# Kernel tuning notes

Measured on AMD Instinct MI355X. Metric: run time of the kernel, lower is better.

## Reference

```python
import jax, jax.numpy as jnp
import numpy as np

N_HEAD = 16
EPS = 1e-6

def setup_inputs() -> dict:
    key = jax.random.key(0)
    ks = jax.random.split(key, 5)
    B, S, D = 2, 2048, 1024
    scale = 0.02
    return {
        "hidden_states": jax.random.normal(ks[0], (B, S, D), dtype=jnp.float32),
        "w_q": jax.random.normal(ks[1], (D, D), dtype=jnp.float32) * scale,
        "w_k": jax.random.normal(ks[2], (D, D), dtype=jnp.float32) * scale,
        "w_v": jax.random.normal(ks[3], (D, D), dtype=jnp.float32) * scale,
        "w_o": jax.random.normal(ks[4], (D, D), dtype=jnp.float32) * scale,
        "qk_norm_factor": jnp.float32(1.0 / np.sqrt(D // N_HEAD)),
    }

def reference(hidden_states, w_q, w_k, w_v, w_o, qk_norm_factor):
    B, S, D = hidden_states.shape
    H = N_HEAD
    hd = D // H
    # projections (torch Linear without bias: x @ W^T)
    q = jnp.einsum('bsd,ed->bse', hidden_states, w_q).reshape(B, S, H, hd).transpose(0, 2, 1, 3)
    k = jnp.einsum('bsd,ed->bse', hidden_states, w_k).reshape(B, S, H, hd).transpose(0, 2, 1, 3)
    v = jnp.einsum('bsd,ed->bse', hidden_states, w_v).reshape(B, S, H, hd).transpose(0, 2, 1, 3)
    # hypersphere (QK) normalization
    q = q / (jnp.linalg.norm(q, axis=-1, keepdims=True) + EPS)
    k = k / (jnp.linalg.norm(k, axis=-1, keepdims=True) + EPS)
    # scores [B,H,S,S], learned scale
    scores = jnp.einsum('bhqd,bhkd->bhqk', q, k) * qk_norm_factor
    causal = jnp.tril(jnp.ones((S, S), dtype=bool))
    scores = jnp.where(causal[None, None], scores, jnp.float32(-jnp.inf))
    probs = jax.nn.softmax(scores, axis=-1)
    attn = jnp.einsum('bhqk,bhkd->bhqd', probs, v)
    attn = attn.transpose(0, 2, 1, 3).reshape(B, S, D)
    out = jnp.einsum('bsd,ed->bse', attn, w_o)
    return out
```

## Files before the change

kernel.cpp:

```cpp
#include <hip/hip_runtime.h>
#include <hip/hip_bf16.h>

typedef __attribute__((ext_vector_type(8))) short short8;
typedef __attribute__((ext_vector_type(4))) float floatx4;

union BF8 { short8 v; __hip_bfloat16 b[8]; };
union BF4U { ushort4 u; __hip_bfloat16 b[4]; };

__device__ __forceinline__ short8 load8(const __hip_bfloat16* p) {
    return *reinterpret_cast<const short8*>(p);
}

__device__ __forceinline__ void storeC(float* p, float v) { *p = v; }
__device__ __forceinline__ void storeC(__hip_bfloat16* p, float v) { *p = __float2bfloat16(v); }

__device__ __forceinline__ unsigned pack_bf16(float a, float b) {
    unsigned ua = __float_as_uint(a) + 0x8000u;
    unsigned ub = __float_as_uint(b) + 0x8000u;
    return __builtin_amdgcn_perm(ub, ua, 0x07060302u);
}

__device__ __forceinline__ float exp2_fast(float x) {
#if __has_builtin(__builtin_amdgcn_exp2f)
    return __builtin_amdgcn_exp2f(x);
#else
    return __expf(x * 0.6931471805599453f);
#endif
}

__device__ __forceinline__ void gload_lds16(const __hip_bfloat16* g, __hip_bfloat16* l) {
    __builtin_amdgcn_global_load_lds(
        (const __attribute__((address_space(1))) void*)g,
        (__attribute__((address_space(3))) void*)l, 16, 0, 0);
}

__global__ __launch_bounds__(256) void cast_all(const float* __restrict__ hs,
                                                const float* __restrict__ wq,
                                                const float* __restrict__ wk,
                                                const float* __restrict__ wv,
                                                const float* __restrict__ wo,
                                                __hip_bfloat16* __restrict__ Xb,
                                                __hip_bfloat16* __restrict__ Wb) {
    int i = blockIdx.x * 256 + threadIdx.x;
    const float* src;
    __hip_bfloat16* dst;
    if (blockIdx.y == 0) {
        src = hs; dst = Xb;
    } else {
        int m = i >> 18;
        src = (m == 0) ? wq : (m == 1) ? wk : (m == 2) ? wv : wo;
        src -= (size_t)m * 1048576;
        dst = Wb;
    }
    float4 v = reinterpret_cast<const float4*>(src)[i];
    BF4U u;
    u.b[0] = __float2bfloat16(v.x);
    u.b[1] = __float2bfloat16(v.y);
    u.b[2] = __float2bfloat16(v.z);
    u.b[3] = __float2bfloat16(v.w);
    reinterpret_cast<ushort4*>(dst)[i] = u.u;
}

template <typename OutT>
__global__ __launch_bounds__(256) void gemm_bt(const __hip_bfloat16* __restrict__ A,
                                               const __hip_bfloat16* __restrict__ B0,
                                               OutT* __restrict__ C0,
                                               int N, int Kd,
                                               size_t zsB, size_t zsC,
                                               int normz, const float* __restrict__ scale_p) {
    __shared__ __hip_bfloat16 lA[128 * 32];
    __shared__ __hip_bfloat16 lB[128 * 32];
    const __hip_bfloat16* B = B0 + zsB * blockIdx.z;
    OutT* C = C0 + zsC * blockIdx.z;
    const int t = threadIdx.x;
    const int m0 = blockIdx.x * 128, n0 = blockIdx.y * 128;
    const int w = t >> 6, l = t & 63;
    const int wr = (w >> 1) * 64, wc = (w & 1) * 64;
    const int lr = l & 15, lq = l >> 4;

    const floatx4 zero4 = {0.f, 0.f, 0.f, 0.f};
    floatx4 acc[4][4];
#pragma unroll
    for (int mt = 0; mt < 4; ++mt)
#pragma unroll
        for (int nt = 0; nt < 4; ++nt) acc[mt][nt] = zero4;

    for (int k0 = 0; k0 < Kd; k0 += 32) {
#pragma unroll
        for (int i = 0; i < 2; ++i) {
            int flat = t + i * 256;
            int row = flat >> 2, ch = flat & 3;
            gload_lds16(A + (size_t)(m0 + row) * Kd + k0 + ch * 8, lA + flat * 8);
            gload_lds16(B + (size_t)(n0 + row) * Kd + k0 + ch * 8, lB + flat * 8);
        }
        __syncthreads();
        short8 af[4], bfr[4];
#pragma unroll
        for (int mt = 0; mt < 4; ++mt)
            af[mt] = load8(lA + (wr + mt * 16 + lr) * 32 + lq * 8);
#pragma unroll
        for (int nt = 0; nt < 4; ++nt)
            bfr[nt] = load8(lB + (wc + nt * 16 + lr) * 32 + lq * 8);
#pragma unroll
        for (int mt = 0; mt < 4; ++mt)
#pragma unroll
            for (int nt = 0; nt < 4; ++nt)
                acc[mt][nt] = __builtin_amdgcn_mfma_f32_16x16x32_bf16(
                    af[mt], bfr[nt], acc[mt][nt], 0, 0, 0);
        __syncthreads();
    }

    if (normz && blockIdx.z < 2) {
        const float fac = (blockIdx.z == 0) ? (*scale_p * 1.44269504f) : 1.0f;
#pragma unroll
        for (int mt = 0; mt < 4; ++mt)
#pragma unroll
            for (int r = 0; r < 4; ++r) {
                float ss = 0.f;
#pragma unroll
                for (int nt = 0; nt < 4; ++nt) {
                    float v = acc[mt][nt][r];
                    ss += v * v;
                }
                ss += __shfl_xor(ss, 1, 64);
                ss += __shfl_xor(ss, 2, 64);
                ss += __shfl_xor(ss, 4, 64);
                ss += __shfl_xor(ss, 8, 64);
                float inv = fac / (sqrtf(ss) + 1e-6f);
#pragma unroll
                for (int nt = 0; nt < 4; ++nt) acc[mt][nt][r] *= inv;
            }
    }

#pragma unroll
    for (int mt = 0; mt < 4; ++mt)
#pragma unroll
        for (int nt = 0; nt < 4; ++nt)
#pragma unroll
            for (int r = 0; r < 4; ++r) {
                int row = m0 + wr + mt * 16 + lq * 4 + r;
                int col = n0 + wc + nt * 16 + lr;
                storeC(C + (size_t)row * N + col, acc[mt][nt][r]);
            }
}

__global__ __launch_bounds__(256) void transpose_v(const __hip_bfloat16* __restrict__ V,
                                                   __hip_bfloat16* __restrict__ Vt) {
    const int S = 2048, D = 1024;
    __shared__ __hip_bfloat16 tile[64][72];
    int t = threadIdx.x;
    int s0 = blockIdx.x * 64;
    int bh = blockIdx.y, b = bh >> 4, h = bh & 15;
    const __hip_bfloat16* src = V + ((size_t)b * S) * D + h * 64;
#pragma unroll
    for (int i = 0; i < 2; ++i) {
        int flat = t + i * 256;
        int sr = flat >> 3, ch = flat & 7;
        *reinterpret_cast<short8*>(&tile[sr][ch * 8]) =
            load8(src + (size_t)(s0 + sr) * D + ch * 8);
    }
    __syncthreads();
    __hip_bfloat16* dst = Vt + (size_t)bh * 64 * S;
#pragma unroll
    for (int i = 0; i < 2; ++i) {
        int flat = t + i * 256;
        int d = flat >> 3, sc = flat & 7;
        BF8 u;
#pragma unroll
        for (int j = 0; j < 8; ++j) u.b[j] = tile[sc * 8 + j][d];
        *reinterpret_cast<short8*>(dst + (size_t)d * S + s0 + sc * 8) = u.v;
    }
}

__global__ __launch_bounds__(256) void flash_attn(const __hip_bfloat16* __restrict__ Q,
                                                  const __hip_bfloat16* __restrict__ K,
                                                  const __hip_bfloat16* __restrict__ Vt,
                                                  __hip_bfloat16* __restrict__ O) {
    const int S = 2048, D = 1024;
    __shared__ __align__(16) char smem[20480];
    const int t = threadIdx.x;
    const int w = t >> 6, l = t & 63;
    const int lr = l & 15, lq = l >> 4;
    const int id = blockIdx.x, jj = id >> 3;
    const int bh = (id & 7) * 4 + (jj & 3);
    const int jq = 31 - (jj >> 2);
    const int b = bh >> 4, h = bh & 15;
    const int q0 = jq * 64;
    const __hip_bfloat16* Qb = Q + ((size_t)b * S) * D + h * 64;
    const __hip_bfloat16* Kb = K + ((size_t)b * S) * D + h * 64;
    const __hip_bfloat16* Vb = Vt + (size_t)bh * 64 * S;
    __hip_bfloat16* lPw = reinterpret_cast<__hip_bfloat16*>(smem) + w * (64 * 40);

    short8 bq[4][2];
#pragma unroll
    for (int nt = 0; nt < 4; ++nt)
#pragma unroll
        for (int kt = 0; kt < 2; ++kt)
            bq[nt][kt] = load8(Qb + (size_t)(q0 + nt * 16 + lr) * D + kt * 32 + lq * 8);

    const floatx4 zero4 = {0.f, 0.f, 0.f, 0.f};
    floatx4 oacc[4][4];
    float lsum[4] = {0.f, 0.f, 0.f, 0.f};
#pragma unroll
    for (int mt = 0; mt < 4; ++mt)
#pragma unroll
        for (int nt = 0; nt < 4; ++nt) oacc[mt][nt] = zero4;

    auto body = [&](int k0, bool domask) {
        short8 bk[2][2], bv[4];
#pragma unroll
        for (int mt = 0; mt < 2; ++mt)
#pragma unroll
            for (int kt = 0; kt < 2; ++kt)
                bk[mt][kt] = load8(Kb + (size_t)(k0 + mt * 16 + lr) * D + kt * 32 + lq * 8);
#pragma unroll
        for (int nt = 0; nt < 4; ++nt)
            bv[nt] = load8(Vb + (size_t)(nt * 16 + lr) * S + k0 + lq * 8);
        floatx4 sacc[2][4];
#pragma unroll
        for (int mt = 0; mt < 2; ++mt)
#pragma unroll
            for (int nt = 0; nt < 4; ++nt) sacc[mt][nt] = zero4;
#pragma unroll
        for (int mt = 0; mt < 2; ++mt)
#pragma unroll
            for (int nt = 0; nt < 4; ++nt)
#pragma unroll
                for (int kt = 0; kt < 2; ++kt)
                    sacc[mt][nt] = __builtin_amdgcn_mfma_f32_16x16x32_bf16(
                        bk[mt][kt], bq[nt][kt], sacc[mt][nt], 0, 0, 0);
#pragma unroll
        for (int mt = 0; mt < 2; ++mt)
#pragma unroll
            for (int nt = 0; nt < 4; ++nt) {
                float p0 = exp2_fast(sacc[mt][nt][0]);
                float p1 = exp2_fast(sacc[mt][nt][1]);
                float p2 = exp2_fast(sacc[mt][nt][2]);
                float p3 = exp2_fast(sacc[mt][nt][3]);
                if (domask) {
                    const int qg = q0 + nt * 16 + lr;
                    const int kb = k0 + mt * 16 + lq * 4;
                    p0 = (kb + 0 <= qg) ? p0 : 0.f;
                    p1 = (kb + 1 <= qg) ? p1 : 0.f;
                    p2 = (kb + 2 <= qg) ? p2 : 0.f;
                    p3 = (kb + 3 <= qg) ? p3 : 0.f;
                }
                lsum[nt] += (p0 + p1) + (p2 + p3);
                uint2 d;
                d.x = pack_bf16(p0, p1);
                d.y = pack_bf16(p2, p3);
                *reinterpret_cast<uint2*>(lPw + (nt * 16 + lr) * 40 + mt * 16 + lq * 4) = d;
            }
        asm volatile("s_waitcnt lgkmcnt(0)" ::: "memory");
        short8 ap[4];
#pragma unroll
        for (int mtq = 0; mtq < 4; ++mtq)
            ap[mtq] = load8(lPw + (mtq * 16 + lr) * 40 + lq * 8);
#pragma unroll
        for (int mtq = 0; mtq < 4; ++mtq)
#pragma unroll
            for (int ntd = 0; ntd < 4; ++ntd)
                oacc[mtq][ntd] = __builtin_amdgcn_mfma_f32_16x16x32_bf16(
                    ap[mtq], bv[ntd], oacc[mtq][ntd], 0, 0, 0);
    };

    int ks = w;
    for (; ks < 2 * jq; ks += 4) body(ks * 32, false);
    for (; ks <= 2 * jq + 1; ks += 4) body(ks * 32, true);

#pragma unroll
    for (int nt = 0; nt < 4; ++nt) {
        float s = lsum[nt];
        s += __shfl_xor(s, 16, 64);
        s += __shfl_xor(s, 32, 64);
        lsum[nt] = s;
    }

    float* buf = reinterpret_cast<float*>(smem);
    const int row = t >> 2, c0 = (t & 3) * 4;
    __hip_bfloat16* Ob = O + ((size_t)b * S) * D + h * 64;
    float inv = 0.f;
#pragma unroll
    for (int chunk = 0; chunk < 4; ++chunk) {
#pragma unroll
        for (int mtq = 0; mtq < 4; ++mtq)
#pragma unroll
            for (int r = 0; r < 4; ++r)
                buf[w * 1280 + (mtq * 16 + lq * 4 + r) * 20 + lr] = oacc[mtq][chunk][r];
        if (chunk == 0 && lq == 0) {
#pragma unroll
            for (int nt = 0; nt < 4; ++nt)
                buf[w * 1280 + (nt * 16 + lr) * 20 + 16] = lsum[nt];
        }
        __syncthreads();
        if (chunk == 0) {
            float Lt = buf[row * 20 + 16] + buf[1280 + row * 20 + 16] +
                       buf[2560 + row * 20 + 16] + buf[3840 + row * 20 + 16];
            inv = 1.f / Lt;
        }
        float4 a = {0.f, 0.f, 0.f, 0.f};
#pragma unroll
        for (int w2 = 0; w2 < 4; ++w2) {
            float4 v = *reinterpret_cast<const float4*>(buf + w2 * 1280 + row * 20 + c0);
            a.x += v.x; a.y += v.y; a.z += v.z; a.w += v.w;
        }
        uint2 d;
        d.x = pack_bf16(a.x * inv, a.y * inv);
        d.y = pack_bf16(a.z * inv, a.w * inv);
        *reinterpret_cast<uint2*>(Ob + (size_t)(q0 + row) * D + chunk * 16 + c0) = d;
        if (chunk < 3) __syncthreads();
    }
}

extern "C" void kernel_launch(void* const* d_in, const int* in_sizes, int n_in,
                              void* d_out, int out_size, void* d_ws, size_t ws_size,
                              hipStream_t stream) {
    const float* hs  = (const float*)d_in[0];
    const float* wq  = (const float*)d_in[1];
    const float* wk  = (const float*)d_in[2];
    const float* wv  = (const float*)d_in[3];
    const float* wo  = (const float*)d_in[4];
    const float* qkf = (const float*)d_in[5];

    char* ws = (char*)d_ws;
    const size_t MB = 1024 * 1024;
    __hip_bfloat16* Xb  = (__hip_bfloat16*)(ws);
    __hip_bfloat16* Wqb = (__hip_bfloat16*)(ws + 8 * MB);
    __hip_bfloat16* Wob = (__hip_bfloat16*)(ws + 14 * MB);
    __hip_bfloat16* Qb  = (__hip_bfloat16*)(ws + 16 * MB);
    __hip_bfloat16* Vb  = (__hip_bfloat16*)(ws + 32 * MB);
    __hip_bfloat16* Vt  = (__hip_bfloat16*)(ws + 40 * MB);
    __hip_bfloat16* Ab  = (__hip_bfloat16*)(ws + 48 * MB);
    __hip_bfloat16* Kb  = (__hip_bfloat16*)(ws + 24 * MB);

    cast_all<<<dim3(4096, 2), 256, 0, stream>>>(hs, wq, wk, wv, wo, Xb, Wqb);

    gemm_bt<__hip_bfloat16><<<dim3(32, 8, 3), 256, 0, stream>>>(
        Xb, Wqb, Qb, 1024, 1024, (size_t)1048576, (size_t)4194304, 1, qkf);

    transpose_v<<<dim3(32, 32), 256, 0, stream>>>(Vb, Vt);
    flash_attn<<<1024, 256, 0, stream>>>(Qb, Kb, Vt, Ab);

    gemm_bt<float><<<dim3(32, 8, 1), 256, 0, stream>>>(
        Ab, Wob, (float*)d_out, 1024, 1024, (size_t)0, (size_t)0, 0, qkf);
}
```

Baseline: 197.3 us.

## Pair causal query tiles per block and prefetch next K/V fragments

Each flash-attention block now handles two query tiles, a long one (31-pr) and a short one (pr), so every block does the same amount of causal work. This halves the grid to 512 blocks. The key loop is also software-pipelined: the next iteration's K and V fragments are loaded into registers before the current tile's MFMAs run, hiding global load latency. In exchange it raises register pressure, adds an extra sync per chunk, and leaves fewer blocks to hide latency.

```diff
diff --git a/kernel.cpp b/kernel.cpp
--- a/kernel.cpp
+++ b/kernel.cpp
@@ -181,134 +181,166 @@
     const int t = threadIdx.x;
     const int w = t >> 6, l = t & 63;
     const int lr = l & 15, lq = l >> 4;
-    const int id = blockIdx.x, jj = id >> 3;
-    const int bh = (id & 7) * 4 + (jj & 3);
-    const int jq = 31 - (jj >> 2);
+    const int id = blockIdx.x;
+    const int bh = (id & 7) * 4 + ((id >> 3) & 3);
+    const int pr = id >> 5;
     const int b = bh >> 4, h = bh & 15;
-    const int q0 = jq * 64;
     const __hip_bfloat16* Qb = Q + ((size_t)b * S) * D + h * 64;
     const __hip_bfloat16* Kb = K + ((size_t)b * S) * D + h * 64;
     const __hip_bfloat16* Vb = Vt + (size_t)bh * 64 * S;
     __hip_bfloat16* lPw = reinterpret_cast<__hip_bfloat16*>(smem) + w * (64 * 40);
-
-    short8 bq[4][2];
-#pragma unroll
-    for (int nt = 0; nt < 4; ++nt)
-#pragma unroll
-        for (int kt = 0; kt < 2; ++kt)
-            bq[nt][kt] = load8(Qb + (size_t)(q0 + nt * 16 + lr) * D + kt * 32 + lq * 8);
-
-    const floatx4 zero4 = {0.f, 0.f, 0.f, 0.f};
-    floatx4 oacc[4][4];
-    float lsum[4] = {0.f, 0.f, 0.f, 0.f};
-#pragma unroll
-    for (int mt = 0; mt < 4; ++mt)
-#pragma unroll
-        for (int nt = 0; nt < 4; ++nt) oacc[mt][nt] = zero4;
-
-    auto body = [&](int k0, bool domask) {
-        short8 bk[2][2], bv[4];
-#pragma unroll
-        for (int mt = 0; mt < 2; ++mt)
+    float* buf = reinterpret_cast<float*>(smem);
+
+#pragma unroll 1
+    for (int tile = 0; tile < 2; ++tile) {
+        const int jq = (tile == 0) ? (31 - pr) : pr;
+        const int q0 = jq * 64;
+
+        short8 bq[4][2];
+#pragma unroll
+        for (int nt = 0; nt < 4; ++nt)
 #pragma unroll
             for (int kt = 0; kt < 2; ++kt)
-                bk[mt][kt] = load8(Kb + (size_t)(k0 + mt * 16 + lr) * D + kt * 32 + lq * 8);
-#pragma unroll
-        for (int nt = 0; nt < 4; ++nt)
-            bv[nt] = load8(Vb + (size_t)(nt * 16 + lr) * S + k0 + lq * 8);
-        floatx4 sacc[2][4];
-#pragma unroll
-        for (int mt = 0; mt < 2; ++mt)
-#pragma unroll
-            for (int nt = 0; nt < 4; ++nt) sacc[mt][nt] = zero4;
-#pragma unroll
-        for (int mt = 0; mt < 2; ++mt)
-#pragma unroll
-            for (int nt = 0; nt < 4; ++nt)
-#pragma unroll
-                for (int kt = 0; kt < 2; ++kt)
-                    sacc[mt][nt] = __builtin_amdgcn_mfma_f32_16x16x32_bf16(
-                        bk[mt][kt], bq[nt][kt], sacc[mt][nt], 0, 0, 0);
-#pragma unroll
-        for (int mt = 0; mt < 2; ++mt)
-#pragma unroll
-            for (int nt = 0; nt < 4; ++nt) {
-                float p0 = exp2_fast(sacc[mt][nt][0]);
-                float p1 = exp2_fast(sacc[mt][nt][1]);
-                float p2 = exp2_fast(sacc[mt][nt][2]);
-                float p3 = exp2_fast(sacc[mt][nt][3]);
-                if (domask) {
-                    const int qg = q0 + nt * 16 + lr;
-                    const int kb = k0 + mt * 16 + lq * 4;
-                    p0 = (kb + 0 <= qg) ? p0 : 0.f;
-                    p1 = (kb + 1 <= qg) ? p1 : 0.f;
-                    p2 = (kb + 2 <= qg) ? p2 : 0.f;
-                    p3 = (kb + 3 <= qg) ? p3 : 0.f;
-                }
-                lsum[nt] += (p0 + p1) + (p2 + p3);
-                uint2 d;
-                d.x = pack_bf16(p0, p1);
-                d.y = pack_bf16(p2, p3);
-                *reinterpret_cast<uint2*>(lPw + (nt * 16 + lr) * 40 + mt * 16 + lq * 4) = d;
-            }
-        asm volatile("s_waitcnt lgkmcnt(0)" ::: "memory");
-        short8 ap[4];
-#pragma unroll
-        for (int mtq = 0; mtq < 4; ++mtq)
-            ap[mtq] = load8(lPw + (mtq * 16 + lr) * 40 + lq * 8);
-#pragma unroll
-        for (int mtq = 0; mtq < 4; ++mtq)
-#pragma unroll
-            for (int ntd = 0; ntd < 4; ++ntd)
-                oacc[mtq][ntd] = __builtin_amdgcn_mfma_f32_16x16x32_bf16(
-                    ap[mtq], bv[ntd], oacc[mtq][ntd], 0, 0, 0);
-    };
-
-    int ks = w;
-    for (; ks < 2 * jq; ks += 4) body(ks * 32, false);
-    for (; ks <= 2 * jq + 1; ks += 4) body(ks * 32, true);
-
-#pragma unroll
-    for (int nt = 0; nt < 4; ++nt) {
-        float s = lsum[nt];
-        s += __shfl_xor(s, 16, 64);
-        s += __shfl_xor(s, 32, 64);
-        lsum[nt] = s;
-    }
-
-    float* buf = reinterpret_cast<float*>(smem);
-    const int row = t >> 2, c0 = (t & 3) * 4;
-    __hip_bfloat16* Ob = O + ((size_t)b * S) * D + h * 64;
-    float inv = 0.f;
-#pragma unroll
-    for (int chunk = 0; chunk < 4; ++chunk) {
-#pragma unroll
-        for (int mtq = 0; mtq < 4; ++mtq)
-#pragma unroll
-            for (int r = 0; r < 4; ++r)
-                buf[w * 1280 + (mtq * 16 + lq * 4 + r) * 20 + lr] = oacc[mtq][chunk][r];
-        if (chunk == 0 && lq == 0) {
-#pragma unroll
-            for (int nt = 0; nt < 4; ++nt)
-                buf[w * 1280 + (nt * 16 + lr) * 20 + 16] = lsum[nt];
+                bq[nt][kt] = load8(Qb + (size_t)(q0 + nt * 16 + lr) * D + kt * 32 + lq * 8);
+
+        const floatx4 zero4 = {0.f, 0.f, 0.f, 0.f};
+        floatx4 oacc[4][4];
+        float lsum[4] = {0.f, 0.f, 0.f, 0.f};
+#pragma unroll
+        for (int mt = 0; mt < 4; ++mt)
+#pragma unroll
+            for (int nt = 0; nt < 4; ++nt) oacc[mt][nt] = zero4;
+
+        const int klast = 2 * jq + 1;
+        const int kmask = 2 * jq;
+
+        if (w <= klast) {
+            short8 bk[2][2], bv[4];
+            {
+                const int k0 = w * 32;
+#pragma unroll
+                for (int mt = 0; mt < 2; ++mt)
+#pragma unroll
+                    for (int kt = 0; kt < 2; ++kt)
+                        bk[mt][kt] = load8(Kb + (size_t)(k0 + mt * 16 + lr) * D + kt * 32 + lq * 8);
+#pragma unroll
+                for (int nt = 0; nt < 4; ++nt)
+                    bv[nt] = load8(Vb + (size_t)(nt * 16 + lr) * S + k0 + lq * 8);
+            }
+            int ks = w;
+#pragma unroll 1
+            while (true) {
+                const int k0 = ks * 32;
+                const bool more = (ks + 4) <= klast;
+                const int k0n = (more ? (ks + 4) : ks) * 32;
+                short8 nk[2][2], nv[4];
+#pragma unroll
+                for (int mt = 0; mt < 2; ++mt)
+#pragma unroll
+                    for (int kt = 0; kt < 2; ++kt)
+                        nk[mt][kt] = load8(Kb + (size_t)(k0n + mt * 16 + lr) * D + kt * 32 + lq * 8);
+#pragma unroll
+                for (int nt = 0; nt < 4; ++nt)
+                    nv[nt] = load8(Vb + (size_t)(nt * 16 + lr) * S + k0n + lq * 8);
+                floatx4 sacc[2][4];
+#pragma unroll
+                for (int mt = 0; mt < 2; ++mt)
+#pragma unroll
+                    for (int nt = 0; nt < 4; ++nt) sacc[mt][nt] = zero4;
+#pragma unroll
+                for (int mt = 0; mt < 2; ++mt)
+#pragma unroll
+                    for (int nt = 0; nt < 4; ++nt)
+#pragma unroll
+                        for (int kt = 0; kt < 2; ++kt)
+                            sacc[mt][nt] = __builtin_amdgcn_mfma_f32_16x16x32_bf16(
+                                bk[mt][kt], bq[nt][kt], sacc[mt][nt], 0, 0, 0);
+                const bool domask = ks >= kmask;
+#pragma unroll
+                for (int mt = 0; mt < 2; ++mt)
+#pragma unroll
+                    for (int nt = 0; nt < 4; ++nt) {
+                        float p0 = exp2_fast(sacc[mt][nt][0]);
+                        float p1 = exp2_fast(sacc[mt][nt][1]);
+                        float p2 = exp2_fast(sacc[mt][nt][2]);
+                        float p3 = exp2_fast(sacc[mt][nt][3]);
+                        if (domask) {
+                            const int qg = q0 + nt * 16 + lr;
+                            const int kb = k0 + mt * 16 + lq * 4;
+                            p0 = (kb + 0 <= qg) ? p0 : 0.f;
+                            p1 = (kb + 1 <= qg) ? p1 : 0.f;
+                            p2 = (kb + 2 <= qg) ? p2 : 0.f;
+                            p3 = (kb + 3 <= qg) ? p3 : 0.f;
+                        }
+                        lsum[nt] += (p0 + p1) + (p2 + p3);
+                        uint2 d;
+                        d.x = pack_bf16(p0, p1);
+                        d.y = pack_bf16(p2, p3);
+                        *reinterpret_cast<uint2*>(lPw + (nt * 16 + lr) * 40 + mt * 16 + lq * 4) = d;
+                    }
+                asm volatile("s_waitcnt lgkmcnt(0)" ::: "memory");
+                short8 ap[4];
+#pragma unroll
+                for (int mtq = 0; mtq < 4; ++mtq)
+                    ap[mtq] = load8(lPw + (mtq * 16 + lr) * 40 + lq * 8);
+#pragma unroll
+                for (int mtq = 0; mtq < 4; ++mtq)
+#pragma unroll
+                    for (int ntd = 0; ntd < 4; ++ntd)
+                        oacc[mtq][ntd] = __builtin_amdgcn_mfma_f32_16x16x32_bf16(
+                            ap[mtq], bv[ntd], oacc[mtq][ntd], 0, 0, 0);
+                if (!more) break;
+                ks += 4;
+#pragma unroll
+                for (int mt = 0; mt < 2; ++mt)
+#pragma unroll
+                    for (int kt = 0; kt < 2; ++kt) bk[mt][kt] = nk[mt][kt];
+#pragma unroll
+                for (int nt = 0; nt < 4; ++nt) bv[nt] = nv[nt];
+            }
         }
-        __syncthreads();
-        if (chunk == 0) {
-            float Lt = buf[row * 20 + 16] + buf[1280 + row * 20 + 16] +
-                       buf[2560 + row * 20 + 16] + buf[3840 + row * 20 + 16];
-            inv = 1.f / Lt;
+
+#pragma unroll
+        for (int nt = 0; nt < 4; ++nt) {
+            float s = lsum[nt];
+            s += __shfl_xor(s, 16, 64);
+            s += __shfl_xor(s, 32, 64);
+            lsum[nt] = s;
         }
-        float4 a = {0.f, 0.f, 0.f, 0.f};
-#pragma unroll
-        for (int w2 = 0; w2 < 4; ++w2) {
-            float4 v = *reinterpret_cast<const float4*>(buf + w2 * 1280 + row * 20 + c0);
-            a.x += v.x; a.y += v.y; a.z += v.z; a.w += v.w;
+
+        const int row = t >> 2, c0 = (t & 3) * 4;
+        __hip_bfloat16* Ob = O + ((size_t)b * S) * D + h * 64;
+        float inv = 0.f;
+#pragma unroll 1
+        for (int chunk = 0; chunk < 4; ++chunk) {
+#pragma unroll
+            for (int mtq = 0; mtq < 4; ++mtq)
+#pragma unroll
+                for (int r = 0; r < 4; ++r)
+                    buf[w * 1280 + (mtq * 16 + lq * 4 + r) * 20 + lr] = oacc[mtq][chunk][r];
+            if (chunk == 0 && lq == 0) {
+#pragma unroll
+                for (int nt = 0; nt < 4; ++nt)
+                    buf[w * 1280 + (nt * 16 + lr) * 20 + 16] = lsum[nt];
+            }
+            __syncthreads();
+            if (chunk == 0) {
+                float Lt = buf[row * 20 + 16] + buf[1280 + row * 20 + 16] +
+                           buf[2560 + row * 20 + 16] + buf[3840 + row * 20 + 16];
+                inv = 1.f / Lt;
+            }
+            float4 a = {0.f, 0.f, 0.f, 0.f};
+#pragma unroll
+            for (int w2 = 0; w2 < 4; ++w2) {
+                float4 v = *reinterpret_cast<const float4*>(buf + w2 * 1280 + row * 20 + c0);
+                a.x += v.x; a.y += v.y; a.z += v.z; a.w += v.w;
+            }
+            uint2 d;
+            d.x = pack_bf16(a.x * inv, a.y * inv);
+            d.y = pack_bf16(a.z * inv, a.w * inv);
+            *reinterpret_cast<uint2*>(Ob + (size_t)(q0 + row) * D + chunk * 16 + c0) = d;
+            __syncthreads();
         }
-        uint2 d;
-        d.x = pack_bf16(a.x * inv, a.y * inv);
-        d.y = pack_bf16(a.z * inv, a.w * inv);
-        *reinterpret_cast<uint2*>(Ob + (size_t)(q0 + row) * D + chunk * 16 + c0) = d;
-        if (chunk < 3) __syncthreads();
     }
 }
 
@@ -328,10 +360,10 @@
     __hip_bfloat16* Wqb = (__hip_bfloat16*)(ws + 8 * MB);
     __hip_bfloat16* Wob = (__hip_bfloat16*)(ws + 14 * MB);
     __hip_bfloat16* Qb  = (__hip_bfloat16*)(ws + 16 * MB);
+    __hip_bfloat16* Kb  = (__hip_bfloat16*)(ws + 24 * MB);
     __hip_bfloat16* Vb  = (__hip_bfloat16*)(ws + 32 * MB);
     __hip_bfloat16* Vt  = (__hip_bfloat16*)(ws + 40 * MB);
     __hip_bfloat16* Ab  = (__hip_bfloat16*)(ws + 48 * MB);
-    __hip_bfloat16* Kb  = (__hip_bfloat16*)(ws + 24 * MB);
 
     cast_all<<<dim3(4096, 2), 256, 0, stream>>>(hs, wq, wk, wv, wo, Xb, Wqb);
 
@@ -339,7 +371,7 @@
         Xb, Wqb, Qb, 1024, 1024, (size_t)1048576, (size_t)4194304, 1, qkf);
 
     transpose_v<<<dim3(32, 32), 256, 0, stream>>>(Vb, Vt);
-    flash_attn<<<1024, 256, 0, stream>>>(Qb, Kb, Vt, Ab);
+    flash_attn<<<512, 256, 0, stream>>>(Qb, Kb, Vt, Ab);
 
     gemm_bt<float><<<dim3(32, 8, 1), 256, 0, stream>>>(
         Ab, Wob, (float*)d_out, 1024, 1024, (size_t)0, (size_t)0, 0, qkf);
```

Result: slower. 224.9 us (+14.0%).
